# Performance work log

Measured on AMD Instinct MI355X. Metric: run time of the kernel, lower is better.

## Reference

```python
import jax, jax.numpy as jnp
import numpy as np
import math

N, C, L, D = 8, 16, 1024, 7   # x: [N, in_heads=C, L, in_features=D]
H = 16                        # out_heads
SZ = C * D                    # 112 (in_sz == out_sz since in_heads == out_heads)

def setup_inputs() -> dict:
    key = jax.random.key(0)
    ks = jax.random.split(key, 7)
    s = 1.0 / math.sqrt(SZ)
    return {
        "x":  jax.random.normal(ks[0], (N, C, L, D), dtype=jnp.float32),
        "Wq": jax.random.normal(ks[1], (SZ, SZ), dtype=jnp.float32) * s,
        "bq": jax.random.normal(ks[2], (SZ,), dtype=jnp.float32) * s,
        "Wk": jax.random.normal(ks[3], (SZ, SZ), dtype=jnp.float32) * s,
        "bk": jax.random.normal(ks[4], (SZ,), dtype=jnp.float32) * s,
        "Wv": jax.random.normal(ks[5], (SZ, SZ), dtype=jnp.float32) * s,
        "bv": jax.random.normal(ks[6], (SZ,), dtype=jnp.float32) * s,
    }

def _split_heads(t):
    # [N, L, H*d] -> [N, H, L, d]
    n, l, _ = t.shape
    return t.reshape(n, l, H, -1).transpose(0, 2, 1, 3)

def reference(x, Wq, bq, Wk, bk, Wv, bv):
    n, c, l, d = x.shape
    # [N, C, L, D] -> [N, L, C*D]
    xf = x.transpose(0, 2, 1, 3).reshape(n, l, c * d)
    q = _split_heads(xf @ Wq.T + bq)   # [N, H, L, d]
    k = _split_heads(xf @ Wk.T + bk)
    v = _split_heads(xf @ Wv.T + bv)
    scores = jnp.einsum('bhqd,bhkd->bhqk', q, k)
    # NOTE: original scales by sqrt(scores.shape[-1]) == sqrt(L), not sqrt(head_dim)
    scores = scores / jnp.sqrt(jnp.asarray(l, scores.dtype))
    weights = jax.nn.softmax(scores.astype(jnp.float32), axis=-1).astype(scores.dtype)
    # dropout p=0.5 is identity in eval mode
    return jnp.einsum('bhqk,bhkd->bhqd', weights, v)
```

## Files before the change

### kernel.cpp

```cpp
#include <hip/hip_runtime.h>
#include <math.h>

#define NB 8
#define CH 16
#define LL 1024
#define DD 7
#define HH 16

typedef float    v2f  __attribute__((ext_vector_type(2)));
typedef float    v4f  __attribute__((ext_vector_type(4)));
typedef float    v16f __attribute__((ext_vector_type(16)));
typedef short    v8s  __attribute__((ext_vector_type(8)));
typedef unsigned v4u  __attribute__((ext_vector_type(4)));

#if __has_builtin(__builtin_amdgcn_exp2f)
#define EXP2F(x) __builtin_amdgcn_exp2f(x)
#else
#define EXP2F(x) exp2f(x)
#endif

__device__ inline unsigned bf16_rne(float f) {
    unsigned u = __builtin_bit_cast(unsigned, f);
    return (u + 0x7fffu + ((u >> 16) & 1u)) >> 16;
}
__device__ inline unsigned pack_trunc(float a, float b) {
    unsigned ua = __builtin_bit_cast(unsigned, a);
    unsigned ub = __builtin_bit_cast(unsigned, b);
    return (ua >> 16) | (ub & 0xffff0000u);
}

__global__ __launch_bounds__(256, 2) void qkv_proj(
    const float* __restrict__ x,
    const float* __restrict__ Wq, const float* __restrict__ bq,
    const float* __restrict__ Wk, const float* __restrict__ bk,
    const float* __restrict__ Wv, const float* __restrict__ bv,
    unsigned short* __restrict__ qkvb)
{
    __shared__ __align__(16) float Ws[112 * 112];
    __shared__ __align__(16) float xt[64 * 116];

    int bx  = blockIdx.x;
    int mat = bx / (NB * 16);
    int rem = bx % (NB * 16);
    int n   = rem / 16;
    int l0  = (rem % 16) * 64;

    const float* W = (mat == 0) ? Wq : (mat == 1) ? Wk : Wv;
    const float* b = (mat == 0) ? bq : (mat == 1) ? bk : bv;

    int tid = threadIdx.x;

    {
        const uint4* src = (const uint4*)W;
        uint4* dst = (uint4*)Ws;
        for (int i = tid; i < 3136; i += 256) dst[i] = src[i];
    }
    for (int idx = tid; idx < 64 * 112; idx += 256) {
        int c  = idx / 448;
        int r  = idx - c * 448;
        int l  = r / 7;
        int dd = r - l * 7;
        xt[l * 116 + c * 7 + dd] = x[((n * CH + c) * LL + l0 + l) * DD + dd];
    }
    __syncthreads();

    int jh = tid >> 4;
    int lg = tid & 15;

    v2f acc2[2][7];
    #pragma unroll
    for (int j = 0; j < 7; ++j) {
        float bj = b[jh * 7 + j];
        acc2[0][j] = (v2f){bj, bj};
        acc2[1][j] = (v2f){bj, bj};
    }

    const v4f* Wv4 = (const v4f*)Ws;
    const v4f* Xv4 = (const v4f*)xt;

    for (int i4 = 0; i4 < 28; ++i4) {
        v4f wv[7];
        #pragma unroll
        for (int j = 0; j < 7; ++j) wv[j] = Wv4[(jh * 7 + j) * 28 + i4];
        v4f x0 = Xv4[(0  + lg) * 29 + i4];
        v4f x1 = Xv4[(16 + lg) * 29 + i4];
        v4f x2 = Xv4[(32 + lg) * 29 + i4];
        v4f x3 = Xv4[(48 + lg) * 29 + i4];
        #pragma unroll
        for (int f = 0; f < 4; ++f) {
            v2f xa = (v2f){x0[f], x1[f]};
            v2f xb = (v2f){x2[f], x3[f]};
            #pragma unroll
            for (int j = 0; j < 7; ++j) {
                v2f wj = (v2f){wv[j][f], wv[j][f]};
                acc2[0][j] += xa * wj;
                acc2[1][j] += xb * wj;
            }
        }
    }

    const float scale = (mat == 0) ? 0.0450842200277801f  : 1.0f;
    #pragma unroll
    for (int rp = 0; rp < 2; ++rp) {
        #pragma unroll
        for (int e = 0; e < 2; ++e) {
            int r = rp * 2 + e;
            float a0 = acc2[rp][0][e] * scale, a1 = acc2[rp][1][e] * scale;
            float a2 = acc2[rp][2][e] * scale, a3 = acc2[rp][3][e] * scale;
            float a4 = acc2[rp][4][e] * scale, a5 = acc2[rp][5][e] * scale;
            float a6 = acc2[rp][6][e] * scale;
            unsigned d0 = bf16_rne(a0) | (bf16_rne(a1) << 16);
            unsigned d1 = bf16_rne(a2) | (bf16_rne(a3) << 16);
            unsigned d2 = bf16_rne(a4) | (bf16_rne(a5) << 16);
            unsigned d3 = bf16_rne(a6);
            int row = l0 + r * 16 + lg;
            uint4* dst = (uint4*)qkvb + ((size_t)(mat * NB + n) * HH + jh) * LL + row;
            *dst = make_uint4(d0, d1, d2, d3);
        }
    }
}

__global__ __launch_bounds__(256, 4) void attn(
    const unsigned short* __restrict__ qkvb, float* __restrict__ out)
{
    __shared__ __align__(16) unsigned short Kl[LL * 8];
    __shared__ __align__(16) unsigned short Vt[8 * 1048];

    int bx = blockIdx.x;
    int qt = bx & 7, h = (bx >> 3) & 15, n = bx >> 7;
    int tid  = threadIdx.x;
    int wave = tid >> 6, lane = tid & 63;
    int l31 = lane & 31, g5 = lane >> 5;

    const unsigned short* Qg = qkvb + (size_t)((0 * NB + n) * HH + h) * (LL * 8);
    const unsigned short* Kg = qkvb + (size_t)((1 * NB + n) * HH + h) * (LL * 8);
    const unsigned short* Vg = qkvb + (size_t)((2 * NB + n) * HH + h) * (LL * 8);

    {
        const uint4* Ks = (const uint4*)Kg;
        uint4* Kd = (uint4*)Kl;
        #pragma unroll
        for (int it = 0; it < 4; ++it) Kd[tid + it * 256] = Ks[tid + it * 256];
    }
    {
        const uint4* Vs = (const uint4*)Vg;
        uint4 r0 = Vs[4 * tid], r1 = Vs[4 * tid + 1];
        uint4 r2 = Vs[4 * tid + 2], r3 = Vs[4 * tid + 3];
        const unsigned* p0 = (const unsigned*)&r0;
        const unsigned* p1 = (const unsigned*)&r1;
        const unsigned* p2 = (const unsigned*)&r2;
        const unsigned* p3 = (const unsigned*)&r3;
        int col = ((tid >> 3) << 5) + ((tid & 1) << 3) + (((tid >> 1) & 1) << 2)
                + (((tid >> 2) & 1) << 4);
        #pragma unroll
        for (int d = 0; d < 7; ++d) {
            unsigned a0 = p0[d >> 1], a1 = p1[d >> 1], a2 = p2[d >> 1], a3 = p3[d >> 1];
            unsigned w0, w1;
            if (d & 1) { w0 = (a0 >> 16) | (a1 & 0xffff0000u); w1 = (a2 >> 16) | (a3 & 0xffff0000u); }
            else       { w0 = (a0 & 0xffffu) | (a1 << 16);     w1 = (a2 & 0xffffu) | (a3 << 16); }
            *(uint2*)&Vt[d * 1048 + col] = make_uint2(w0, w1);
        }
        *(uint2*)&Vt[7 * 1048 + col] = make_uint2(0x3f803f80u, 0x3f803f80u);
    }
    __syncthreads();

    int q = qt * 128 + wave * 32 + l31;
    v8s zero8 = {0, 0, 0, 0, 0, 0, 0, 0};
    v8s qf = (lane < 32) ? *(const v8s*)(Qg + (size_t)q * 8) : zero8;

    const unsigned short* Vrow = Vt + (l31 & 7) * 1048 + g5 * 8;
    v16f acc = {};

    v8s kf = (lane < 32) ? *(const v8s*)(Kl + l31 * 8) : zero8;

    #pragma unroll 4
    for (int c = 0; c < 32; ++c) {
        v16f s = __builtin_amdgcn_mfma_f32_32x32x16_bf16(kf, qf, (v16f){}, 0, 0, 0);
        if (c < 31)
            kf = (lane < 32) ? *(const v8s*)(Kl + ((c + 1) * 32 + l31) * 8) : zero8;
        v8s va1 = *(const v8s*)(Vrow + c * 32);
        v8s va2 = *(const v8s*)(Vrow + c * 32 + 16);

        unsigned pk[8];
        #pragma unroll
        for (int p = 0; p < 8; ++p)
            pk[p] = pack_trunc(EXP2F(s[2 * p]), EXP2F(s[2 * p + 1]));
        v8s pA = __builtin_bit_cast(v8s, (v4u){pk[0], pk[1], pk[2], pk[3]});
        v8s pB = __builtin_bit_cast(v8s, (v4u){pk[4], pk[5], pk[6], pk[7]});

        acc = __builtin_amdgcn_mfma_f32_32x32x16_bf16(va1, pA, acc, 0, 0, 0);
        acc = __builtin_amdgcn_mfma_f32_32x32x16_bf16(va2, pB, acc, 0, 0, 0);
    }

    float rs = __shfl(acc[3], 32 + l31, 64);
    float* base = out + (size_t)(n * HH + h) * LL * 7 + (size_t)q * 7;
    #pragma unroll
    for (int r = 0; r < 4; ++r) {
        int dim = 4 * g5 + r;
        if (dim < 7) base[dim] = acc[r] / rs;
    }
}

extern "C" void kernel_launch(void* const* d_in, const int* in_sizes, int n_in,
                              void* d_out, int out_size, void* d_ws, size_t ws_size,
                              hipStream_t stream) {
    const float* x  = (const float*)d_in[0];
    const float* Wq = (const float*)d_in[1];
    const float* bq = (const float*)d_in[2];
    const float* Wk = (const float*)d_in[3];
    const float* bk = (const float*)d_in[4];
    const float* Wv = (const float*)d_in[5];
    const float* bv = (const float*)d_in[6];
    unsigned short* qkvb = (unsigned short*)d_ws;
    float* o = (float*)d_out;

    qkv_proj<<<dim3(3 * NB * 16), dim3(256), 0, stream>>>(x, Wq, bq, Wk, bk, Wv, bv, qkvb);
    attn<<<dim3(NB * HH * 8), dim3(256), 0, stream>>>(qkvb, o);
}
```

Baseline: 106.6 us.

## Compute QKV projection with bf16 MFMA instead of fp32 FMA loops

Rewrites the QKV projection kernel so that the weight and x tiles are converted to bf16 in shared memory with zero-padded K, and the 64x112x112 GEMM per block runs through mfma_f32_16x16x32_bf16 instead of scalar fp32 packed FMAs. Outputs are scattered as individual bf16 halfwords, and pad slot 7 is zeroed separately. This is meant to remove the ALU-bound projection cost. In exchange it adds bf16 rounding of the inputs and weights before the matmul, which lowers precision, and it replaces the vector 16-byte stores with uncoalesced 2-byte stores.

```diff
diff --git a/kernel.cpp b/kernel.cpp
--- a/kernel.cpp
+++ b/kernel.cpp
@@ -36,8 +36,8 @@
     const float* __restrict__ Wv, const float* __restrict__ bv,
     unsigned short* __restrict__ qkvb)
 {
-    __shared__ __align__(16) float Ws[112 * 112];
-    __shared__ __align__(16) float xt[64 * 116];
+    __shared__ __align__(16) unsigned short Wb[112 * 136];
+    __shared__ __align__(16) unsigned short xb[64 * 136];
 
     int bx  = blockIdx.x;
     int mat = bx / (NB * 16);
@@ -51,71 +51,73 @@
     int tid = threadIdx.x;
 
     {
-        const uint4* src = (const uint4*)W;
-        uint4* dst = (uint4*)Ws;
-        for (int i = tid; i < 3136; i += 256) dst[i] = src[i];
+        const float4* Wsrc = (const float4*)W;
+        for (int i4 = tid; i4 < 3136; i4 += 256) {
+            int j  = i4 / 28;
+            int ii = (i4 - j * 28) * 4;
+            float4 w = Wsrc[i4];
+            unsigned lo = bf16_rne(w.x) | (bf16_rne(w.y) << 16);
+            unsigned hi = bf16_rne(w.z) | (bf16_rne(w.w) << 16);
+            *(uint2*)&Wb[j * 136 + ii] = make_uint2(lo, hi);
+        }
     }
     for (int idx = tid; idx < 64 * 112; idx += 256) {
         int c  = idx / 448;
         int r  = idx - c * 448;
         int l  = r / 7;
         int dd = r - l * 7;
-        xt[l * 116 + c * 7 + dd] = x[((n * CH + c) * LL + l0 + l) * DD + dd];
+        xb[l * 136 + c * 7 + dd] =
+            (unsigned short)bf16_rne(x[((n * CH + c) * LL + l0 + l) * DD + dd]);
+    }
+    for (int idx = tid; idx < 64 * 16; idx += 256)
+        xb[(idx >> 4) * 136 + 112 + (idx & 15)] = 0;
+    for (int idx = tid; idx < 112 * 16; idx += 256)
+        Wb[(idx >> 4) * 136 + 112 + (idx & 15)] = 0;
+
+    {
+        size_t base = ((size_t)(mat * NB + n) * HH) * (LL * 8);
+        for (int idx = tid; idx < 1024; idx += 256) {
+            int hh = idx >> 6, l = idx & 63;
+            qkvb[base + (size_t)(hh * LL + l0 + l) * 8 + 7] = 0;
+        }
     }
     __syncthreads();
 
-    int jh = tid >> 4;
-    int lg = tid & 15;
-
-    v2f acc2[2][7];
-    #pragma unroll
-    for (int j = 0; j < 7; ++j) {
-        float bj = b[jh * 7 + j];
-        acc2[0][j] = (v2f){bj, bj};
-        acc2[1][j] = (v2f){bj, bj};
-    }
-
-    const v4f* Wv4 = (const v4f*)Ws;
-    const v4f* Xv4 = (const v4f*)xt;
-
-    for (int i4 = 0; i4 < 28; ++i4) {
-        v4f wv[7];
-        #pragma unroll
-        for (int j = 0; j < 7; ++j) wv[j] = Wv4[(jh * 7 + j) * 28 + i4];
-        v4f x0 = Xv4[(0  + lg) * 29 + i4];
-        v4f x1 = Xv4[(16 + lg) * 29 + i4];
-        v4f x2 = Xv4[(32 + lg) * 29 + i4];
-        v4f x3 = Xv4[(48 + lg) * 29 + i4];
-        #pragma unroll
-        for (int f = 0; f < 4; ++f) {
-            v2f xa = (v2f){x0[f], x1[f]};
-            v2f xb = (v2f){x2[f], x3[f]};
-            #pragma unroll
-            for (int j = 0; j < 7; ++j) {
-                v2f wj = (v2f){wv[j][f], wv[j][f]};
-                acc2[0][j] += xa * wj;
-                acc2[1][j] += xb * wj;
-            }
+    int wv = tid >> 6, lane = tid & 63, l15 = lane & 15, l4 = lane >> 4;
+
+    const unsigned short* Arow = xb + (wv * 16 + l15) * 136 + l4 * 8;
+    v8s af[4];
+    #pragma unroll
+    for (int k4 = 0; k4 < 4; ++k4) af[k4] = *(const v8s*)(Arow + k4 * 32);
+
+    v4f acc[7];
+    #pragma unroll
+    for (int jt = 0; jt < 7; ++jt) acc[jt] = (v4f){0.f, 0.f, 0.f, 0.f};
+
+    #pragma unroll
+    for (int jt = 0; jt < 7; ++jt) {
+        const unsigned short* Brow = Wb + (jt * 16 + l15) * 136 + l4 * 8;
+        #pragma unroll
+        for (int k4 = 0; k4 < 4; ++k4) {
+            v8s bf = *(const v8s*)(Brow + k4 * 32);
+            acc[jt] = __builtin_amdgcn_mfma_f32_16x16x32_bf16(af[k4], bf, acc[jt], 0, 0, 0);
         }
     }
 
     const float scale = (mat == 0) ? 0.0450842200277801f  : 1.0f;
-    #pragma unroll
-    for (int rp = 0; rp < 2; ++rp) {
-        #pragma unroll
-        for (int e = 0; e < 2; ++e) {
-            int r = rp * 2 + e;
-            float a0 = acc2[rp][0][e] * scale, a1 = acc2[rp][1][e] * scale;
-            float a2 = acc2[rp][2][e] * scale, a3 = acc2[rp][3][e] * scale;
-            float a4 = acc2[rp][4][e] * scale, a5 = acc2[rp][5][e] * scale;
-            float a6 = acc2[rp][6][e] * scale;
-            unsigned d0 = bf16_rne(a0) | (bf16_rne(a1) << 16);
-            unsigned d1 = bf16_rne(a2) | (bf16_rne(a3) << 16);
-            unsigned d2 = bf16_rne(a4) | (bf16_rne(a5) << 16);
-            unsigned d3 = bf16_rne(a6);
-            int row = l0 + r * 16 + lg;
-            uint4* dst = (uint4*)qkvb + ((size_t)(mat * NB + n) * HH + jh) * LL + row;
-            *dst = make_uint4(d0, d1, d2, d3);
+    size_t mbase = ((size_t)(mat * NB + n) * HH) * (LL * 8);
+    #pragma unroll
+    for (int jt = 0; jt < 7; ++jt) {
+        int j   = jt * 16 + l15;
+        int hh  = j / 7;
+        int dim = j - hh * 7;
+        float bj = b[j];
+        int lrow = l0 + wv * 16 + l4 * 4;
+        size_t rb = mbase + (size_t)hh * (LL * 8) + (size_t)lrow * 8 + dim;
+        #pragma unroll
+        for (int r = 0; r < 4; ++r) {
+            float val = (acc[jt][r] + bj) * scale;
+            qkvb[rb + (size_t)r * 8] = (unsigned short)bf16_rne(val);
         }
     }
 }
```

New measurement: 101.6 us. -4.8%, faster.
